# Performance work log

Measured on AMD Instinct MI355X. Metric: run time of the kernel, lower is better.

## Reference

```python
import jax, jax.numpy as jnp
import numpy as np

# LIF constants from snn_layer.call (single_neuron path)
DT = 0.01
R = 3000.0
C = 0.05          # tau_m = R*C = 150
V_THR = 15.0
V_R = 0.0
V_MAX = 30.0
I_AMP = 150.0     # stimulus 'on' amplitude in stimuli_gen

T, N = 1000, 131072  # timesteps, parallel neurons


def setup_inputs() -> dict:
    key = jax.random.key(0)
    # stimuli in [0, 150): same scale as the original step stimulus
    stimuli = jax.random.uniform(key, (T, N), dtype=jnp.float32) * I_AMP
    return {"stimuli": stimuli}


def reference(stimuli):
    """Sequential LIF Euler integration with threshold reset/spike clamp.

    stimuli: [T, N] input current per timestep per neuron.
    Returns v_trace: [T, N] membrane potential trace (post-update each step),
    matching single_neuron()/solve() semantics:
      1) if v >= V_thr: v = V_r (reset from a previous spike)
         else:          v += ((-v + R*I) / (R*C)) * dt   (Euler step)
      2) if v >= V_thr: v = V_max (spike clamp)
    """
    tm = R * C

    def step(v, i_t):
        v_euler = v + ((-v + R * i_t) / tm) * DT
        v_new = jnp.where(v >= V_THR, V_R, v_euler)
        v_new = jnp.where(v_new >= V_THR, V_MAX, v_new)
        return v_new, v_new

    v0 = jnp.zeros(stimuli.shape[1], dtype=stimuli.dtype)
    _, v_trace = jax.lax.scan(step, v0, stimuli)  # [T, N]
    return v_trace
```

## Files before the change

kernel.cpp:

```cpp
#include <hip/hip_runtime.h>

#define DT_F    0.01f
#define TM_F    150.0f
#define R_F     3000.0f
#define V_THR_F 15.0f
#define V_MAX_F 30.0f

template <int U>
__global__ __launch_bounds__(256) void lif_kernel(const float* __restrict__ stim,
                                                  float* __restrict__ out,
                                                  int T, int N) {
#pragma clang fp contract(off)
    const int n = blockIdx.x * blockDim.x + threadIdx.x;
    if (n >= N) return;

    const float* sp = stim + n;
    float*       op = out + n;

    float v = 0.0f;
    int t = 0;
    for (; t + U <= T; t += U) {
        float s[U];
#pragma unroll
        for (int u = 0; u < U; ++u) {
            s[u] = sp[(size_t)(t + u) * (size_t)N];
        }
#pragma unroll
        for (int u = 0; u < U; ++u) {
            float v_euler = v + ((-v + R_F * s[u]) / TM_F) * DT_F;
            float vn = (v >= V_THR_F) ? 0.0f : v_euler;
            vn = (vn >= V_THR_F) ? V_MAX_F : vn;
            v = vn;
            op[(size_t)(t + u) * (size_t)N] = v;
        }
    }
    for (; t < T; ++t) {
        float s = sp[(size_t)t * (size_t)N];
        float v_euler = v + ((-v + R_F * s) / TM_F) * DT_F;
        float vn = (v >= V_THR_F) ? 0.0f : v_euler;
        vn = (vn >= V_THR_F) ? V_MAX_F : vn;
        v = vn;
        op[(size_t)t * (size_t)N] = v;
    }
}

extern "C" void kernel_launch(void* const* d_in, const int* in_sizes, int n_in,
                              void* d_out, int out_size, void* d_ws, size_t ws_size,
                              hipStream_t stream) {
    const float* stim = (const float*)d_in[0];
    float*       out  = (float*)d_out;

    constexpr int T = 1000;
    constexpr int N = 131072;

    constexpr int BLOCK = 256;
    const int grid = (N + BLOCK - 1) / BLOCK;
    lif_kernel<8><<<grid, BLOCK, 0, stream>>>(stim, out, T, N);
}
```

Baseline: 818.1 us.

## Software-pipeline stimulus loads with a rolling prefetch buffer and nontemporal stores

Result: slower. 836.1 us (+2.2%).

```diff
diff --git a/kernel.cpp b/kernel.cpp
--- a/kernel.cpp
+++ b/kernel.cpp
@@ -6,41 +6,50 @@
 #define V_THR_F 15.0f
 #define V_MAX_F 30.0f
 
-template <int U>
+template <int PF>
 __global__ __launch_bounds__(256) void lif_kernel(const float* __restrict__ stim,
                                                   float* __restrict__ out,
                                                   int T, int N) {
 #pragma clang fp contract(off)
+    static_assert(1000 % PF == 0, "PF must divide T");
     const int n = blockIdx.x * blockDim.x + threadIdx.x;
     if (n >= N) return;
 
-    const float* sp = stim + n;
-    float*       op = out + n;
+    const unsigned stride = (unsigned)N;
+    unsigned ld = (unsigned)n;
+    unsigned st = (unsigned)n;
+
+    float s[PF];
+#pragma unroll
+    for (int u = 0; u < PF; ++u) { s[u] = stim[ld]; ld += stride; }
 
     float v = 0.0f;
-    int t = 0;
-    for (; t + U <= T; t += U) {
-        float s[U];
+    const int rounds = T / PF - 1;
+    for (int r = 0; r < rounds; ++r) {
 #pragma unroll
-        for (int u = 0; u < U; ++u) {
-            s[u] = sp[(size_t)(t + u) * (size_t)N];
-        }
-#pragma unroll
-        for (int u = 0; u < U; ++u) {
-            float v_euler = v + ((-v + R_F * s[u]) / TM_F) * DT_F;
+        for (int u = 0; u < PF; ++u) {
+            float cur = s[u];
+            s[u] = stim[ld]; ld += stride;
+
+            float v_euler = v + ((-v + R_F * cur) / TM_F) * DT_F;
             float vn = (v >= V_THR_F) ? 0.0f : v_euler;
             vn = (vn >= V_THR_F) ? V_MAX_F : vn;
             v = vn;
-            op[(size_t)(t + u) * (size_t)N] = v;
+
+            __builtin_nontemporal_store(v, &out[st]);
+            st += stride;
         }
     }
-    for (; t < T; ++t) {
-        float s = sp[(size_t)t * (size_t)N];
-        float v_euler = v + ((-v + R_F * s) / TM_F) * DT_F;
+
+#pragma unroll
+    for (int u = 0; u < PF; ++u) {
+        float cur = s[u];
+        float v_euler = v + ((-v + R_F * cur) / TM_F) * DT_F;
         float vn = (v >= V_THR_F) ? 0.0f : v_euler;
         vn = (vn >= V_THR_F) ? V_MAX_F : vn;
         v = vn;
-        op[(size_t)t * (size_t)N] = v;
+        __builtin_nontemporal_store(v, &out[st]);
+        st += stride;
     }
 }
 
@@ -55,5 +64,5 @@
 
     constexpr int BLOCK = 256;
     const int grid = (N + BLOCK - 1) / BLOCK;
-    lif_kernel<8><<<grid, BLOCK, 0, stream>>>(stim, out, T, N);
+    lif_kernel<20><<<grid, BLOCK, 0, stream>>>(stim, out, T, N);
 }
```
